# Optimization experiments

Hardware: AMD Instinct MI355X
Metric: run time of the kernel (lower is better)

Reference implementation:

```python
import jax, jax.numpy as jnp
import numpy as np

B, S, F = 512, 512, 128   # batch, seq_len, facts_size (= querry_size)
H1, H2 = 80, 40
PAD = float(-2**32 + 1)


def setup_inputs() -> dict:
    key = jax.random.key(0)
    ks = jax.random.split(key, 12)
    inp = {
        "query": jax.random.normal(ks[0], (B, F), jnp.float32),
        "facts": jax.random.normal(ks[1], (B, S, F), jnp.float32),
        "mask": jax.random.randint(ks[2], (B, S), 0, 2, jnp.int32),
        # mlp1: querry_size -> facts_size
        "W1": jax.random.normal(ks[3], (F, F), jnp.float32) / np.sqrt(F),
        "b1": jnp.zeros((F,), jnp.float32),
        # PReLU alpha (per-feature, init zeros)
        "alpha": jnp.zeros((F,), jnp.float32),
        # mlp2: 4*F -> 80
        "W2": jax.random.normal(ks[4], (4 * F, H1), jnp.float32) / np.sqrt(4 * F),
        "b2": jnp.zeros((H1,), jnp.float32),
        # mlp3: 80 -> 40
        "W3": jax.random.normal(ks[5], (H1, H2), jnp.float32) / np.sqrt(H1),
        "b3": jnp.zeros((H2,), jnp.float32),
        # mlp4: 40 -> 1
        "W4": jax.random.normal(ks[6], (H2, 1), jnp.float32) / np.sqrt(H2),
        "b4": jnp.zeros((1,), jnp.float32),
    }
    return inp


def reference(query, facts, mask, W1, b1, alpha, W2, b2, W3, b3, W4, b4):
    # mlp1 + PReLU on the query
    q = query @ W1 + b1                                   # [B, F]
    q = jnp.where(q >= 0, q, alpha * q)                   # PReLU, alpha per-feature
    # broadcast query over sequence (tile+reshape in the original)
    qs = jnp.broadcast_to(q[:, None, :], (q.shape[0], S, F))  # [B, S, F]
    din = jnp.concatenate([qs, facts, qs - facts, qs * facts], axis=-1)  # [B,S,4F]
    h1 = jax.nn.sigmoid(din @ W2 + b2)                    # [B, S, 80]
    h2 = jax.nn.sigmoid(h1 @ W3 + b3)                     # [B, S, 40]
    scores = (h2 @ W4 + b4)[..., 0][:, None, :]           # [B, 1, S]
    key_masks = (mask == 1)[:, None, :]                   # [B, 1, S]
    scores = jnp.where(key_masks, scores, PAD)
    scores = jax.nn.softmax(scores, axis=-1)              # softmax over seq
    out = jnp.einsum("bqs,bsf->bqf", scores, facts)       # [B, 1, F]  (mode SUM)
    return out
```

## Files before the change

kernel.cpp:

```cpp
#include <hip/hip_runtime.h>
#include <hip/hip_bf16.h>

typedef __bf16 bf16x8 __attribute__((ext_vector_type(8)));
typedef float  f32x4  __attribute__((ext_vector_type(4)));

#define WBT_STRIDE 136
#define H1_STRIDE  104
#define W3T_STRIDE 104

#define LOAD_CT(av, rl)                                                         \
    {                                                                           \
        const float* p0 = &fb[(size_t)(wave * 64 + (rl)) * 128 + qd * 8];       \
        _Pragma("unroll")                                                       \
        for (int kc = 0; kc < 4; ++kc) {                                        \
            av[kc][0] = *(const f32x4*)(p0 + kc * 32);                          \
            av[kc][1] = *(const f32x4*)(p0 + kc * 32 + 4);                      \
        }                                                                       \
    }

#define CONV_AF(af, av)                                                         \
    _Pragma("unroll")                                                           \
    for (int kc = 0; kc < 4; ++kc)                                              \
        _Pragma("unroll")                                                       \
        for (int i = 0; i < 8; ++i)                                             \
            af[kc][i] = (__bf16)((i < 4) ? av[kc][0][i] : av[kc][1][i - 4]);

#define SCORE_CT(af, tile)                                                      \
    {                                                                           \
         \
        _Pragma("unroll")                                                       \
        for (int ct = 0; ct < 5; ++ct) {                                        \
            f32x4 acc = {0.f, 0.f, 0.f, 0.f};                                   \
            _Pragma("unroll")                                                   \
            for (int kc = 0; kc < 4; ++kc) {                                    \
                bf16x8 bfr = *(const bf16x8*)&WbT[(ct * 16 + m) * WBT_STRIDE + kc * 32 + qd * 8]; \
                acc = __builtin_amdgcn_mfma_f32_16x16x32_bf16(af[kc], bfr, acc, 0, 0, 0); \
            }                                                                   \
            const int col = ct * 16 + m;    \
            const float qc = qcs[col];                                          \
            _Pragma("unroll")                                                   \
            for (int r = 0; r < 4; ++r) {                                       \
                float x = acc[r] + qc;                                          \
                float h = __builtin_amdgcn_rcpf(1.0f + __expf(-x));             \
                h1w[(qd * 4 + r) * H1_STRIDE + col] = (__bf16)h;                \
            }                                                                   \
        }                                                                       \
        asm volatile("s_waitcnt lgkmcnt(0)" ::: "memory");    \
                      \
        bf16x8 a2[3];                                                           \
        _Pragma("unroll")                                                       \
        for (int kc = 0; kc < 3; ++kc)                                          \
            a2[kc] = *(const bf16x8*)&h1w[m * H1_STRIDE + kc * 32 + qd * 8];    \
        float sc[4] = {0.f, 0.f, 0.f, 0.f};                                     \
        _Pragma("unroll")                                                       \
        for (int ct = 0; ct < 3; ++ct) {                                        \
            f32x4 acc2 = {0.f, 0.f, 0.f, 0.f};                                  \
            _Pragma("unroll")                                                   \
            for (int kc = 0; kc < 3; ++kc) {                                    \
                bf16x8 bfr = *(const bf16x8*)&W3T[(ct * 16 + m) * W3T_STRIDE + kc * 32 + qd * 8]; \
                acc2 = __builtin_amdgcn_mfma_f32_16x16x32_bf16(a2[kc], bfr, acc2, 0, 0, 0); \
            }                                                                   \
            const int col = ct * 16 + m;                                        \
            const float w4v = w4s[col], b3v = b3s[col];                         \
            _Pragma("unroll")                                                   \
            for (int r = 0; r < 4; ++r) {                                       \
                float h2 = __builtin_amdgcn_rcpf(1.0f + __expf(-(acc2[r] + b3v))); \
                sc[r] = fmaf(h2, w4v, sc[r]);                                   \
            }                                                                   \
        }                                                                       \
        _Pragma("unroll")                                                       \
        for (int d = 1; d < 16; d <<= 1)                                        \
            _Pragma("unroll")                                                   \
            for (int r = 0; r < 4; ++r)                                         \
                sc[r] += __shfl_xor(sc[r], d);                                  \
          \
        float s0v = __int_as_float(__builtin_amdgcn_ds_bpermute(idx, __float_as_int(sc[0]))); \
        float s1v = __int_as_float(__builtin_amdgcn_ds_bpermute(idx, __float_as_int(sc[1]))); \
        float s2v = __int_as_float(__builtin_amdgcn_ds_bpermute(idx, __float_as_int(sc[2]))); \
        float s3v = __int_as_float(__builtin_amdgcn_ds_bpermute(idx, __float_as_int(sc[3]))); \
        const int rr = m & 3;                                                   \
        float srow = (rr == 0) ? s0v : (rr == 1) ? s1v : (rr == 2) ? s2v : s3v; \
        const float pmv = (((tile) * 16 + m) < cnt) ? __expf(srow) : 0.f;       \
        Zl += pmv;                                                              \
        if (qd == 0) pmall[wave * 64 + (tile) * 16 + m] = pmv;                  \
    }

__global__ __launch_bounds__(512, 2)
void attn_fused(const float* __restrict__ query,
                const float* __restrict__ facts,
                const int*   __restrict__ mask,
                const float* __restrict__ W1, const float* __restrict__ b1,
                const float* __restrict__ alpha,
                const float* __restrict__ W2, const float* __restrict__ b2,
                const float* __restrict__ W3, const float* __restrict__ b3,
                const float* __restrict__ W4,
                float* __restrict__ out)
{
    __shared__ __align__(16) __bf16 WbT[80 * WBT_STRIDE];
    __shared__ __align__(16) __bf16 W3T[48 * W3T_STRIDE];
    __shared__ __align__(16) __bf16 h1all[128 * H1_STRIDE];
    __shared__ float qy[128], qs[128], qcs[80];
    __shared__ float qpart[4][128], qcp[4][80];
    __shared__ float w4s[48], b3s[48];
    __shared__ float outw[8 * 128];
    __shared__ float pmall[8 * 64];
    __shared__ unsigned char cidx8[8 * 64];
    __shared__ float Zw[8];

    const int b = blockIdx.x, t = threadIdx.x;
    const int wave = t >> 6, lane = t & 63, qd = lane >> 4, m = lane & 15;
    const float* fb = facts + (size_t)b * (512 * 128);
    const int*   mb = mask + b * 512;

    const int mvl = mb[wave * 64 + lane];
    const unsigned long long bal = __ballot(mvl == 1);
    const int cnt = __popcll(bal);
    cidx8[wave * 64 + lane] = 0;
    asm volatile("s_waitcnt lgkmcnt(0)" ::: "memory");
    if (mvl == 1) {
        const int rank = __popcll(bal & ((1ull << lane) - 1ull));
        cidx8[wave * 64 + rank] = (unsigned char)lane;
    }
    asm volatile("s_waitcnt lgkmcnt(0)" ::: "memory");
    const int rl0 = cidx8[wave * 64 +  0 + m];
    const int rl1 = cidx8[wave * 64 + 16 + m];
    const int rl2 = cidx8[wave * 64 + 32 + m];
    const int rl3 = cidx8[wave * 64 + 48 + m];

    f32x4 av[4][2];
    LOAD_CT(av, rl0)

    if (t < 128) qy[t] = query[b * 128 + t];
    for (int e = t; e < 48 * 96; e += 512) {
        int j = e / 96, k = e % 96;
        W3T[j * W3T_STRIDE + k] = (j < 40 && k < 80) ? (__bf16)W3[k * 40 + j]
                                                     : (__bf16)0.0f;
    }
    for (int e = t; e < 128 * 16; e += 512) {
        int r = e >> 4, c = 80 + (e & 15);
        h1all[r * H1_STRIDE + c] = (__bf16)0.0f;
    }
    if (t < 48) { w4s[t] = (t < 40) ? W4[t] : 0.f; b3s[t] = (t < 40) ? b3[t] : 0.f; }
    __syncthreads();

    {
        int j = t & 127, kh = t >> 7;
        float acc = (kh == 0) ? b1[j] : 0.f;
        const float* w1p = W1 + (kh * 32) * 128 + j;
        #pragma unroll 8
        for (int k = 0; k < 32; ++k) acc = fmaf(qy[kh * 32 + k], w1p[k * 128], acc);
        qpart[kh][j] = acc;
    }
    __syncthreads();
    if (t < 128) {
        float s = (qpart[0][t] + qpart[1][t]) + (qpart[2][t] + qpart[3][t]);
        qs[t] = (s >= 0.f) ? s : alpha[t] * s;
    }
    __syncthreads();

    if (t < 320) {
        int jj = t % 80, hh = t / 80;
        float acc = (hh == 0) ? b2[jj] : 0.f;
        #pragma unroll 8
        for (int k = hh * 32; k < hh * 32 + 32; ++k)
            acc = fmaf(qs[k], W2[k * 80 + jj] + W2[(256 + k) * 80 + jj], acc);
        qcp[hh][jj] = acc;
    }
    for (int e = t; e < 128 * 80; e += 512) {
        int k = e / 80, n = e - k * 80;
        float w = W2[(128 + k) * 80 + n] - W2[(256 + k) * 80 + n]
                + qs[k] * W2[(384 + k) * 80 + n];
        WbT[n * WBT_STRIDE + k] = (__bf16)w;
    }
    __syncthreads();
    if (t < 80) qcs[t] = (qcp[0][t] + qcp[1][t]) + (qcp[2][t] + qcp[3][t]);
    __syncthreads();

    __bf16* h1w = &h1all[wave * 16 * H1_STRIDE];
    const int idx = ((((m >> 2) << 4) | m) << 2);

    float Zl = 0.f;
    bf16x8 af[4];

    CONV_AF(af, av)
    if (cnt > 16) LOAD_CT(av, rl1)
    SCORE_CT(af, 0)
    if (cnt > 16) {
        CONV_AF(af, av)
        if (cnt > 32) LOAD_CT(av, rl2)
        SCORE_CT(af, 1)
    }
    if (cnt > 32) {
        CONV_AF(af, av)
        if (cnt > 48) LOAD_CT(av, rl3)
        SCORE_CT(af, 2)
    }
    if (cnt > 48) {
        CONV_AF(af, av)
        SCORE_CT(af, 3)
    }

    asm volatile("s_waitcnt lgkmcnt(0)" ::: "memory");
    float oA = 0.f, oB = 0.f;
    {
        const float* fw = fb + (size_t)(wave * 64) * 128;
        const float* pmw = &pmall[wave * 64];
        const unsigned char* ci = &cidx8[wave * 64];
        #pragma unroll 4
        for (int j = 0; j < cnt; ++j) {
            const float p = pmw[j];
            const int rl = ci[j];
            oA = fmaf(p, fw[rl * 128 + lane], oA);
            oB = fmaf(p, fw[rl * 128 + 64 + lane], oB);
        }
        outw[wave * 128 + lane] = oA;
        outw[wave * 128 + 64 + lane] = oB;
    }

    #pragma unroll
    for (int d = 1; d < 16; d <<= 1) Zl += __shfl_xor(Zl, d);
    if (lane == 0) Zw[wave] = Zl;
    __syncthreads();

    if (t < 128) {
        float v = 0.f, Z = 0.f;
        #pragma unroll
        for (int w = 0; w < 8; ++w) { v += outw[w * 128 + t]; Z += Zw[w]; }
        out[b * 128 + t] = v / Z;
    }
}

extern "C" void kernel_launch(void* const* d_in, const int* in_sizes, int n_in,
                              void* d_out, int out_size, void* d_ws, size_t ws_size,
                              hipStream_t stream) {
    (void)in_sizes; (void)n_in; (void)d_ws; (void)ws_size; (void)out_size;
    const float* query = (const float*)d_in[0];
    const float* facts = (const float*)d_in[1];
    const int*   mask  = (const int*)d_in[2];
    const float* W1 = (const float*)d_in[3];
    const float* b1 = (const float*)d_in[4];
    const float* al = (const float*)d_in[5];
    const float* W2 = (const float*)d_in[6];
    const float* b2 = (const float*)d_in[7];
    const float* W3 = (const float*)d_in[8];
    const float* b3 = (const float*)d_in[9];
    const float* W4 = (const float*)d_in[10];
    const float* b4 = (const float*)d_in[11];
    (void)b4;
    attn_fused<<<dim3(512), dim3(512), 0, stream>>>(
        query, facts, mask, W1, b1, al, W2, b2, W3, b3, W4, (float*)d_out);
}
```

Before: 219.3 us.

## Accumulate weighted facts from registers and prefetch all fact tiles upfront

The final softmax-weighted sum no longer re-reads the facts rows from global memory. Each lane now reuses the fp32 fact values it already holds in registers for the MFMA operands, multiplying them by the row's exp score and reducing across the 16 row lanes with shuffles. All four per-wave fact tiles are also issued as loads at kernel start rather than one tile ahead. This removes a second pass over facts and the pmall staging buffer, at the cost of many more live registers (four tile buffers plus a 32-float accumulator) and a larger cross-lane shuffle reduction, which may hurt occupancy under the 512x2 launch bounds.

```diff
diff --git a/kernel.cpp b/kernel.cpp
--- a/kernel.cpp
+++ b/kernel.cpp
@@ -25,7 +25,7 @@
         for (int i = 0; i < 8; ++i)                                             \
             af[kc][i] = (__bf16)((i < 4) ? av[kc][0][i] : av[kc][1][i - 4]);
 
-#define SCORE_CT(af, tile)                                                      \
+#define SCORE_ACC_CT(af, av, tile)                                              \
     {                                                                           \
          \
         _Pragma("unroll")                                                       \
@@ -80,9 +80,16 @@
         float s3v = __int_as_float(__builtin_amdgcn_ds_bpermute(idx, __float_as_int(sc[3]))); \
         const int rr = m & 3;                                                   \
         float srow = (rr == 0) ? s0v : (rr == 1) ? s1v : (rr == 2) ? s2v : s3v; \
+         \
         const float pmv = (((tile) * 16 + m) < cnt) ? __expf(srow) : 0.f;       \
         Zl += pmv;                                                              \
-        if (qd == 0) pmall[wave * 64 + (tile) * 16 + m] = pmv;                  \
+        _Pragma("unroll")                                                       \
+        for (int kc = 0; kc < 4; ++kc)                                          \
+            _Pragma("unroll")                                                   \
+            for (int i = 0; i < 4; ++i) {                                       \
+                oacc[kc][i]     = fmaf(pmv, av[kc][0][i], oacc[kc][i]);         \
+                oacc[kc][i + 4] = fmaf(pmv, av[kc][1][i], oacc[kc][i + 4]);     \
+            }                                                                   \
     }
 
 __global__ __launch_bounds__(512, 2)
@@ -103,7 +110,6 @@
     __shared__ float qpart[4][128], qcp[4][80];
     __shared__ float w4s[48], b3s[48];
     __shared__ float outw[8 * 128];
-    __shared__ float pmall[8 * 64];
     __shared__ unsigned char cidx8[8 * 64];
     __shared__ float Zw[8];
 
@@ -127,8 +133,11 @@
     const int rl2 = cidx8[wave * 64 + 32 + m];
     const int rl3 = cidx8[wave * 64 + 48 + m];
 
-    f32x4 av[4][2];
-    LOAD_CT(av, rl0)
+    f32x4 av0[4][2], av1[4][2], av2[4][2], av3[4][2];
+    LOAD_CT(av0, rl0)
+    if (cnt > 16) LOAD_CT(av1, rl1)
+    if (cnt > 32) LOAD_CT(av2, rl2)
+    if (cnt > 48) LOAD_CT(av3, rl3)
 
     if (t < 128) qy[t] = query[b * 128 + t];
     for (int e = t; e < 48 * 96; e += 512) {
@@ -180,46 +189,45 @@
     const int idx = ((((m >> 2) << 4) | m) << 2);
 
     float Zl = 0.f;
+    float oacc[4][8];
+    #pragma unroll
+    for (int kc = 0; kc < 4; ++kc)
+        #pragma unroll
+        for (int i = 0; i < 8; ++i) oacc[kc][i] = 0.f;
     bf16x8 af[4];
 
-    CONV_AF(af, av)
-    if (cnt > 16) LOAD_CT(av, rl1)
-    SCORE_CT(af, 0)
+    CONV_AF(af, av0)
+    SCORE_ACC_CT(af, av0, 0)
     if (cnt > 16) {
-        CONV_AF(af, av)
-        if (cnt > 32) LOAD_CT(av, rl2)
-        SCORE_CT(af, 1)
+        CONV_AF(af, av1)
+        SCORE_ACC_CT(af, av1, 1)
     }
     if (cnt > 32) {
-        CONV_AF(af, av)
-        if (cnt > 48) LOAD_CT(av, rl3)
-        SCORE_CT(af, 2)
+        CONV_AF(af, av2)
+        SCORE_ACC_CT(af, av2, 2)
     }
     if (cnt > 48) {
-        CONV_AF(af, av)
-        SCORE_CT(af, 3)
-    }
-
-    asm volatile("s_waitcnt lgkmcnt(0)" ::: "memory");
-    float oA = 0.f, oB = 0.f;
-    {
-        const float* fw = fb + (size_t)(wave * 64) * 128;
-        const float* pmw = &pmall[wave * 64];
-        const unsigned char* ci = &cidx8[wave * 64];
-        #pragma unroll 4
-        for (int j = 0; j < cnt; ++j) {
-            const float p = pmw[j];
-            const int rl = ci[j];
-            oA = fmaf(p, fw[rl * 128 + lane], oA);
-            oB = fmaf(p, fw[rl * 128 + 64 + lane], oB);
-        }
-        outw[wave * 128 + lane] = oA;
-        outw[wave * 128 + 64 + lane] = oB;
+        CONV_AF(af, av3)
+        SCORE_ACC_CT(af, av3, 3)
     }
 
     #pragma unroll
-    for (int d = 1; d < 16; d <<= 1) Zl += __shfl_xor(Zl, d);
-    if (lane == 0) Zw[wave] = Zl;
+    for (int d = 1; d < 16; d <<= 1) {
+        #pragma unroll
+        for (int kc = 0; kc < 4; ++kc)
+            #pragma unroll
+            for (int i = 0; i < 8; ++i)
+                oacc[kc][i] += __shfl_xor(oacc[kc][i], d);
+        Zl += __shfl_xor(Zl, d);
+    }
+    if (m == 0) {
+        #pragma unroll
+        for (int kc = 0; kc < 4; ++kc)
+            #pragma unroll
+            for (int i = 0; i < 8; ++i)
+                outw[wave * 128 + kc * 32 + qd * 8 + i] = oacc[kc][i];
+        if (lane == 0) Zw[wave] = Zl;
+    }
     __syncthreads();
 
     if (t < 128) {
```

Measured after the change: 231.5 us. +5.6%, slower.
